# Performance work log

Measured on AMD Instinct MI355X. Metric: run time of the kernel, lower is better.

## Reference

```python
import jax, jax.numpy as jnp
import numpy as np

N_NODES = 50000
N_EDGES = 800000
F_IN = 128
HEADS = 8
HID = 16
EDGE_DIM = 2
EPS = 1e-5
GAT_SLOPE = 0.2   # GATv2Conv default negative_slope
ACT_SLOPE = 0.01  # GATLayer alpha


def setup_inputs() -> dict:
    key = jax.random.key(0)
    ks = jax.random.split(key, 10)
    HC = HEADS * HID
    return {
        "x": jax.random.normal(ks[0], (N_NODES, F_IN), jnp.float32),
        "edge_idx": jax.random.randint(ks[1], (2, N_EDGES), 0, N_NODES, jnp.int32),
        "edge_attr": jax.random.normal(ks[2], (N_EDGES, EDGE_DIM), jnp.float32),
        "Wl": jax.random.normal(ks[3], (F_IN, HC), jnp.float32) * (1.0 / np.sqrt(F_IN)),
        "bl": jnp.zeros((HC,), jnp.float32),
        "Wr": jax.random.normal(ks[4], (F_IN, HC), jnp.float32) * (1.0 / np.sqrt(F_IN)),
        "br": jnp.zeros((HC,), jnp.float32),
        "We": jax.random.normal(ks[5], (EDGE_DIM, HC), jnp.float32) * (1.0 / np.sqrt(EDGE_DIM)),
        "be": jnp.zeros((HC,), jnp.float32),
        "att": jax.random.normal(ks[6], (HEADS, HID), jnp.float32) * (1.0 / np.sqrt(HID)),
        "bias": jnp.zeros((HC,), jnp.float32),
        "gamma": jnp.ones((HC,), jnp.float32),
        "beta": jnp.zeros((HC,), jnp.float32),
    }


def reference(x, edge_idx, edge_attr, Wl, bl, Wr, br, We, be, att, bias, gamma, beta):
    N = x.shape[0]
    H, C = att.shape
    # GATv2: separate source/target linear maps (share_weights=False)
    xl = (x @ Wl + bl).reshape(N, H, C)      # source transform (messages)
    xr = (x @ Wr + br).reshape(N, H, C)      # target transform
    e = (edge_attr @ We + be).reshape(-1, H, C)
    src, dst = edge_idx[0], edge_idx[1]       # edge j -> i
    # edge-wise attention input: [E, H, C]
    m = jax.nn.leaky_relu(xl[src] + xr[dst] + e, GAT_SLOPE)
    logits = jnp.einsum('ehc,hc->eh', m, att)  # [E, H]
    # segment softmax over incoming edges of each target node
    lmax = jax.ops.segment_max(logits, dst, num_segments=N)          # [N, H]
    ex = jnp.exp(logits - lmax[dst])
    denom = jax.ops.segment_sum(ex, dst, num_segments=N)             # [N, H]
    alpha = ex / denom[dst]                                          # [E, H]
    # weighted scatter-aggregate of source messages, concat heads
    out = jax.ops.segment_sum(xl[src] * alpha[:, :, None], dst, num_segments=N)
    out = out.reshape(N, H * C) + bias
    # BatchNorm over nodes (batch statistics), then LeakyReLU(0.01)
    mean = out.mean(axis=0)
    var = out.var(axis=0)
    out = (out - mean) / jnp.sqrt(var + EPS) * gamma + beta
    return jax.nn.leaky_relu(out, ACT_SLOPE)
```

## Files before the change

kernel.cpp:

```cpp
#include <hip/hip_runtime.h>
#include <hip/hip_bf16.h>

#define N_NODES 50000
#define N_EDGES 800000
#define HEADS 8
#define HID 16
#define HC 128

typedef __attribute__((ext_vector_type(8))) short bf16x8;
typedef __attribute__((ext_vector_type(4))) float f32x4;
typedef __attribute__((ext_vector_type(2))) float f32x2;
typedef __attribute__((ext_vector_type(4))) int i32x4;

__device__ __forceinline__ float bf2f(unsigned short u) {
  union { unsigned int i; float f; } v;
  v.i = (unsigned int)u << 16;
  return v.f;
}
__device__ __forceinline__ unsigned short f2bf(float f) {
  __hip_bfloat16 h = __float2bfloat16(f);
  return *(unsigned short*)&h;
}

template <int CTRL>
__device__ __forceinline__ float dpp_addf(float x) {
  const int r = __builtin_amdgcn_update_dpp(0, __float_as_int(x), CTRL, 0xF, 0xF, true);
  return x + __int_as_float(r);
}

__global__ __launch_bounds__(256) void k_prep(
    const int* __restrict__ eidx, const float* __restrict__ Wl,
    const float* __restrict__ Wr, int* __restrict__ deg,
    unsigned short* __restrict__ WcatT) {
  const int b = blockIdx.x;
  if (b < 3125) {
    const int e = b * 256 + threadIdx.x;
    const int d = __builtin_nontemporal_load(eidx + N_EDGES + e);
    atomicAdd(&deg[d], 1);
  } else {
    const int idx = (b - 3125) * 256 + threadIdx.x;
    const int n = idx >> 7, k = idx & 127;
    const float* W = (n < 128) ? Wl : Wr;
    WcatT[idx] = f2bf(W[k * HC + (n & 127)]);
  }
}

__global__ __launch_bounds__(512) void k_gemm_alloc(
    const float* __restrict__ x, const unsigned short* __restrict__ WcatT,
    const float* __restrict__ bl, const float* __restrict__ br,
    unsigned short* __restrict__ xl, unsigned short* __restrict__ xr,
    const int* __restrict__ deg, int* __restrict__ counter,
    int* __restrict__ offs) {
  __shared__ unsigned short As[128 * 136];
  const int t = threadIdx.x;

  if (blockIdx.x >= 391) {
    const int node = (blockIdx.x - 391) * 512 + t;
    const int lane = t & 63;
    const int v = (node < N_NODES) ? deg[node] : 0;
    int incl = v;
#pragma unroll
    for (int d = 1; d < 64; d <<= 1) {
      const int tt = __shfl_up(incl, d);
      if (lane >= d) incl += tt;
    }
    const int total = __shfl(incl, 63);
    int base = 0;
    if (lane == 63) base = atomicAdd(counter, total);
    base = __shfl(base, 63);
    if (node < N_NODES) offs[node] = base + incl - v;
    return;
  }

  const int m0 = blockIdx.x * 128;
#pragma unroll
  for (int it = 0; it < 4; ++it) {
    const int c = t + it * 512;
    const int row = c >> 4;
    const int seg = (c & 15) * 8;
    const int grow = m0 + row;
    float4 a = make_float4(0.f, 0.f, 0.f, 0.f), bb2 = a;
    if (grow < N_NODES) {
      const float4* p = (const float4*)(x + (size_t)grow * 128 + seg);
      a = p[0];
      bb2 = p[1];
    }
    union { unsigned short s[8]; uint4 v; } o;
    o.s[0] = f2bf(a.x);   o.s[1] = f2bf(a.y);
    o.s[2] = f2bf(a.z);   o.s[3] = f2bf(a.w);
    o.s[4] = f2bf(bb2.x); o.s[5] = f2bf(bb2.y);
    o.s[6] = f2bf(bb2.z); o.s[7] = f2bf(bb2.w);
    *(uint4*)(&As[row * 136 + seg]) = o.v;
  }
  __syncthreads();

  const int w = t >> 6, lane = t & 63;
  const int wm = w >> 2, wn = w & 3;
  const int lr = lane & 15, lk = lane >> 4;

  f32x4 acc[4][4];
#pragma unroll
  for (int i = 0; i < 4; ++i)
#pragma unroll
    for (int j = 0; j < 4; ++j) acc[i][j] = (f32x4)(0.f);

  const unsigned short* Wbase = WcatT + (size_t)(wn * 64 + lr) * 128;
#pragma unroll
  for (int ks = 0; ks < 4; ++ks) {
    const int k = ks * 32 + lk * 8;
    bf16x8 bfr[4], afr[4];
#pragma unroll
    for (int ni = 0; ni < 4; ++ni)
      bfr[ni] = *(const bf16x8*)(Wbase + ni * 16 * 128 + k);
#pragma unroll
    for (int mi = 0; mi < 4; ++mi)
      afr[mi] = *(const bf16x8*)(&As[(wm * 64 + mi * 16 + lr) * 136 + k]);
#pragma unroll
    for (int mi = 0; mi < 4; ++mi)
#pragma unroll
      for (int ni = 0; ni < 4; ++ni)
        acc[mi][ni] = __builtin_amdgcn_mfma_f32_16x16x32_bf16(
            afr[mi], bfr[ni], acc[mi][ni], 0, 0, 0);
  }

#pragma unroll
  for (int ni = 0; ni < 4; ++ni) {
    const int gcol = wn * 64 + ni * 16 + lr;
    const bool left = gcol < 128;
    const float bb = left ? bl[gcol] : br[gcol - 128];
    unsigned short* __restrict__ dst = left ? xl : xr;
    const int cc = gcol & 127;
#pragma unroll
    for (int mi = 0; mi < 4; ++mi) {
#pragma unroll
      for (int r = 0; r < 4; ++r) {
        const int grow = m0 + wm * 64 + mi * 16 + lk * 4 + r;
        if (grow < N_NODES) dst[(size_t)grow * HC + cc] = f2bf(acc[mi][ni][r] + bb);
      }
    }
  }
}

__global__ __launch_bounds__(256) void k_scatter(
    const int* __restrict__ eidx, const float* __restrict__ eattr,
    const int* __restrict__ offs, int* __restrict__ cursor,
    i32x4* __restrict__ epack) {
  const int e = blockIdx.x * 256 + threadIdx.x;
  const int src = __builtin_nontemporal_load(eidx + e);
  const int d = __builtin_nontemporal_load(eidx + N_EDGES + e);
  const f32x2 ea = __builtin_nontemporal_load((const f32x2*)eattr + e);
  const int pos = atomicAdd(&cursor[d], 1);
  i32x4 rec;
  rec.x = src;
  rec.y = __float_as_int(ea.x);
  rec.z = __float_as_int(ea.y);
  rec.w = 0;
  __builtin_nontemporal_store(rec, epack + offs[d] + pos);
}

#define LOADB(EP, K)                                   \
  _Pragma("unroll") for (int j = 0; j < 4; ++j) EP[j] = \
      __builtin_nontemporal_load(epack + (K) + j);
#define LOADX(XW, EP)                                                        \
  _Pragma("unroll") for (int j = 0; j < 4; ++j)                              \
      XW[j] = *(const unsigned int*)((const char*)xl +                       \
              (((unsigned)EP[j].x << 8) + lb));
#define EDGE1(EPJ, XWJ)                                                     \
  {                                                                         \
    const float eax = __int_as_float((EPJ).y);                              \
    const float eay = __int_as_float((EPJ).z);                              \
    const float x0 = bf2f((unsigned short)(XWJ));                           \
    const float x1 = bf2f((unsigned short)((XWJ) >> 16));                   \
    float m0 = fmaf(eax, w0a, fmaf(eay, w1a, ca)) + x0;                     \
    float m1 = fmaf(eax, w0b, fmaf(eay, w1b, cb)) + x1;                     \
    m0 = fmaxf(m0, 0.2f * m0);                                              \
    m1 = fmaxf(m1, 0.2f * m1);                                              \
    float p = fmaf(m0, ata, m1 * atb);                                      \
    p = dpp_addf<0xB1>(p);                                                  \
    p = dpp_addf<0x4E>(p);                                                  \
    p = dpp_addf<0x141>(p);                                                 \
    const float exv = __expf(p);                                            \
    dn += exv;                                                              \
    a0 = fmaf(exv, x0, a0);                                                 \
    a1 = fmaf(exv, x1, a1);                                                 \
  }
#define COMPUTE4(EP, XW)                               \
  _Pragma("unroll") for (int j = 0; j < 4; ++j) EDGE1(EP[j], XW[j])

__global__ __launch_bounds__(256) void k_attagg(
    const int* __restrict__ offs, const int* __restrict__ deg,
    const i32x4* __restrict__ epack,
    const unsigned short* __restrict__ xl, const unsigned short* __restrict__ xr,
    const float* __restrict__ We, const float* __restrict__ be,
    const float* __restrict__ att, float* __restrict__ outp,
    float* __restrict__ statsB) {
  __shared__ float ssum[4 * 128];
  __shared__ float ssq[4 * 128];
  const int wave = threadIdx.x >> 6, lane = threadIdx.x & 63;
  const int node = blockIdx.x * 4 + wave;
  const int c0 = lane * 2;
  const unsigned lb = (unsigned)lane << 2;

  const float w0a = We[c0],      w0b = We[c0 + 1];
  const float w1a = We[HC + c0], w1b = We[HC + c0 + 1];
  const float ata = att[c0],     atb = att[c0 + 1];

  const unsigned int xrw =
      __builtin_nontemporal_load((const unsigned int*)(xr + (size_t)node * HC) + lane);
  const float ca = be[c0] + bf2f((unsigned short)xrw);
  const float cb = be[c0 + 1] + bf2f((unsigned short)(xrw >> 16));

  const int beg = offs[node];
  const int dn_e = deg[node];
  const int end = beg + dn_e;
  const int nf = dn_e >> 2;

  float dn = 0.f, a0 = 0.f, a1 = 0.f;

  if (nf >= 1) {
    i32x4 epA[4], epB[4];
    unsigned int xwA[4];
    LOADB(epA, beg)
    LOADX(xwA, epA)
    if (nf >= 2) LOADB(epB, beg + 4)
    for (int b = 0; b + 1 < nf; ++b) {
      unsigned int xwB[4];
      i32x4 epC[4];
      LOADX(xwB, epB)
      if (b + 2 < nf) LOADB(epC, beg + (b + 2) * 4)
      COMPUTE4(epA, xwA)
#pragma unroll
      for (int j = 0; j < 4; ++j) { epA[j] = epB[j]; xwA[j] = xwB[j]; epB[j] = epC[j]; }
    }
    COMPUTE4(epA, xwA)
  }
  for (int k = beg + (nf << 2); k < end; ++k) {
    const i32x4 ep = __builtin_nontemporal_load(epack + k);
    const unsigned int xw =
        *(const unsigned int*)((const char*)xl + (((unsigned)ep.x << 8) + lb));
    EDGE1(ep, xw)
  }

  const float inv = dn > 0.f ? 1.0f / dn : 0.f;
  const float o0 = a0 * inv, o1 = a1 * inv;
  f32x2 o;
  o.x = o0;
  o.y = o1;
  __builtin_nontemporal_store(o, (f32x2*)(outp + (size_t)node * HC) + lane);

  ssum[wave * 128 + c0]     = o0;
  ssum[wave * 128 + c0 + 1] = o1;
  ssq[wave * 128 + c0]      = o0 * o0;
  ssq[wave * 128 + c0 + 1]  = o1 * o1;
  __syncthreads();
  if (threadIdx.x < 128) {
    const int c = threadIdx.x;
    const float s1 = ssum[c] + ssum[128 + c] + ssum[256 + c] + ssum[384 + c];
    const float s2 = ssq[c] + ssq[128 + c] + ssq[256 + c] + ssq[384 + c];
    float* bkt = statsB + (blockIdx.x & 7) * 256;
    atomicAdd(&bkt[c], s1);
    atomicAdd(&bkt[128 + c], s2);
  }
}

__global__ __launch_bounds__(256) void k_bn(const float* __restrict__ statsB,
                                            const float* __restrict__ gamma,
                                            const float* __restrict__ beta,
                                            float* __restrict__ outp) {
  __shared__ float sscale[128], sshift[128];
  const int t = threadIdx.x;
  if (t < 128) {
    float s1 = 0.f, s2 = 0.f;
#pragma unroll
    for (int b = 0; b < 8; ++b) {
      s1 += statsB[b * 256 + t];
      s2 += statsB[b * 256 + 128 + t];
    }
    const float mean = s1 * (1.0f / N_NODES);
    const float var = s2 * (1.0f / N_NODES) - mean * mean;
    const float rstd = rsqrtf(var + 1e-5f);
    const float sc = rstd * gamma[t];
    sscale[t] = sc;
    sshift[t] = beta[t] - mean * sc;
  }
  __syncthreads();
  const size_t base = (size_t)blockIdx.x * 1024 + t * 4;
  float4 v = *(const float4*)(outp + base);
  const int c = (t * 4) & 127;
  v.x = fmaf(v.x, sscale[c],     sshift[c]);
  v.y = fmaf(v.y, sscale[c + 1], sshift[c + 1]);
  v.z = fmaf(v.z, sscale[c + 2], sshift[c + 2]);
  v.w = fmaf(v.w, sscale[c + 3], sshift[c + 3]);
  v.x = fmaxf(v.x, 0.01f * v.x);
  v.y = fmaxf(v.y, 0.01f * v.y);
  v.z = fmaxf(v.z, 0.01f * v.z);
  v.w = fmaxf(v.w, 0.01f * v.w);
  *(float4*)(outp + base) = v;
}

extern "C" void kernel_launch(void* const* d_in, const int* in_sizes, int n_in,
                              void* d_out, int out_size, void* d_ws, size_t ws_size,
                              hipStream_t stream) {
  const float* x     = (const float*)d_in[0];
  const int*   eidx  = (const int*)d_in[1];
  const float* eattr = (const float*)d_in[2];
  const float* Wl    = (const float*)d_in[3];
  const float* bl    = (const float*)d_in[4];
  const float* Wr    = (const float*)d_in[5];
  const float* br    = (const float*)d_in[6];
  const float* We    = (const float*)d_in[7];
  const float* be    = (const float*)d_in[8];
  const float* att   = (const float*)d_in[9];
  const float* gamma = (const float*)d_in[11];
  const float* beta  = (const float*)d_in[12];
  float* out = (float*)d_out;

  char* ws = (char*)d_ws;
  size_t off = 0;
  auto alloc = [&](size_t bytes) {
    size_t o = off;
    off = (off + bytes + 15) & ~size_t(15);
    return o;
  };
  const size_t o_deg   = alloc((size_t)(N_NODES + 1) * 4);
  const size_t o_cur   = alloc((size_t)N_NODES * 4);
  const size_t o_cnt   = alloc(16);
  const size_t o_stats = alloc((size_t)8 * 256 * 4);
  const size_t zero_bytes = off;
  const size_t o_offs = alloc((size_t)(N_NODES + 1) * 4);
  const size_t o_ep   = alloc((size_t)N_EDGES * 16);
  const size_t o_wt   = alloc((size_t)256 * 128 * 2);
  const size_t o_xl   = alloc((size_t)N_NODES * HC * 2);
  const size_t o_xr   = alloc((size_t)N_NODES * HC * 2);
  (void)ws_size; (void)in_sizes; (void)n_in; (void)out_size;

  int*   deg    = (int*)(ws + o_deg);
  int*   cur    = (int*)(ws + o_cur);
  int*   cnt    = (int*)(ws + o_cnt);
  float* statsB = (float*)(ws + o_stats);
  int*   offs   = (int*)(ws + o_offs);
  i32x4* epack  = (i32x4*)(ws + o_ep);
  unsigned short* WcatT = (unsigned short*)(ws + o_wt);
  unsigned short* xl    = (unsigned short*)(ws + o_xl);
  unsigned short* xr    = (unsigned short*)(ws + o_xr);

  hipMemsetAsync(ws, 0, zero_bytes, stream);

  k_prep<<<3253, 256, 0, stream>>>(eidx, Wl, Wr, deg, WcatT);
  k_gemm_alloc<<<489, 512, 0, stream>>>(x, WcatT, bl, br, xl, xr, deg, cnt, offs);
  k_scatter<<<3125, 256, 0, stream>>>(eidx, eattr, offs, cur, epack);
  k_attagg<<<12500, 256, 0, stream>>>(offs, deg, epack, xl, xr, We, be, att, out,
                                      statsB);
  k_bn<<<6250, 256, 0, stream>>>(statsB, gamma, beta, out);
}
```

Measured before the change: 299.5 us.

## Pack edge records to 8 bytes with bf16 attrs, deepen gather prefetch, use exp2

```diff
diff --git a/kernel.cpp b/kernel.cpp
--- a/kernel.cpp
+++ b/kernel.cpp
@@ -10,7 +10,7 @@
 typedef __attribute__((ext_vector_type(8))) short bf16x8;
 typedef __attribute__((ext_vector_type(4))) float f32x4;
 typedef __attribute__((ext_vector_type(2))) float f32x2;
-typedef __attribute__((ext_vector_type(4))) int i32x4;
+typedef __attribute__((ext_vector_type(2))) int i32x2;
 
 __device__ __forceinline__ float bf2f(unsigned short u) {
   union { unsigned int i; float f; } v;
@@ -144,17 +144,15 @@
 __global__ __launch_bounds__(256) void k_scatter(
     const int* __restrict__ eidx, const float* __restrict__ eattr,
     const int* __restrict__ offs, int* __restrict__ cursor,
-    i32x4* __restrict__ epack) {
+    i32x2* __restrict__ epack) {
   const int e = blockIdx.x * 256 + threadIdx.x;
   const int src = __builtin_nontemporal_load(eidx + e);
   const int d = __builtin_nontemporal_load(eidx + N_EDGES + e);
   const f32x2 ea = __builtin_nontemporal_load((const f32x2*)eattr + e);
   const int pos = atomicAdd(&cursor[d], 1);
-  i32x4 rec;
+  i32x2 rec;
   rec.x = src;
-  rec.y = __float_as_int(ea.x);
-  rec.z = __float_as_int(ea.y);
-  rec.w = 0;
+  rec.y = (int)((unsigned)f2bf(ea.x) | ((unsigned)f2bf(ea.y) << 16));
   __builtin_nontemporal_store(rec, epack + offs[d] + pos);
 }
 
@@ -167,8 +165,9 @@
               (((unsigned)EP[j].x << 8) + lb));
 #define EDGE1(EPJ, XWJ)                                                     \
   {                                                                         \
-    const float eax = __int_as_float((EPJ).y);                              \
-    const float eay = __int_as_float((EPJ).z);                              \
+    const unsigned eu = (unsigned)(EPJ).y;                                  \
+    const float eax = bf2f((unsigned short)eu);                             \
+    const float eay = bf2f((unsigned short)(eu >> 16));                     \
     const float x0 = bf2f((unsigned short)(XWJ));                           \
     const float x1 = bf2f((unsigned short)((XWJ) >> 16));                   \
     float m0 = fmaf(eax, w0a, fmaf(eay, w1a, ca)) + x0;                     \
@@ -179,17 +178,19 @@
     p = dpp_addf<0xB1>(p);                                                  \
     p = dpp_addf<0x4E>(p);                                                  \
     p = dpp_addf<0x141>(p);                                                 \
-    const float exv = __expf(p);                                            \
+    const float exv = exp2f(p);                                             \
     dn += exv;                                                              \
     a0 = fmaf(exv, x0, a0);                                                 \
     a1 = fmaf(exv, x1, a1);                                                 \
   }
 #define COMPUTE4(EP, XW)                               \
   _Pragma("unroll") for (int j = 0; j < 4; ++j) EDGE1(EP[j], XW[j])
+#define SHIFT4(A, B)                                   \
+  _Pragma("unroll") for (int j = 0; j < 4; ++j) A[j] = B[j];
 
 __global__ __launch_bounds__(256) void k_attagg(
     const int* __restrict__ offs, const int* __restrict__ deg,
-    const i32x4* __restrict__ epack,
+    const i32x2* __restrict__ epack,
     const unsigned short* __restrict__ xl, const unsigned short* __restrict__ xr,
     const float* __restrict__ We, const float* __restrict__ be,
     const float* __restrict__ att, float* __restrict__ outp,
@@ -203,7 +204,8 @@
 
   const float w0a = We[c0],      w0b = We[c0 + 1];
   const float w1a = We[HC + c0], w1b = We[HC + c0 + 1];
-  const float ata = att[c0],     atb = att[c0 + 1];
+  const float LOG2E = 1.4426950408889634f;
+  const float ata = att[c0] * LOG2E, atb = att[c0 + 1] * LOG2E;
 
   const unsigned int xrw =
       __builtin_nontemporal_load((const unsigned int*)(xr + (size_t)node * HC) + lane);
@@ -218,24 +220,27 @@
   float dn = 0.f, a0 = 0.f, a1 = 0.f;
 
   if (nf >= 1) {
-    i32x4 epA[4], epB[4];
-    unsigned int xwA[4];
-    LOADB(epA, beg)
-    LOADX(xwA, epA)
-    if (nf >= 2) LOADB(epB, beg + 4)
-    for (int b = 0; b + 1 < nf; ++b) {
-      unsigned int xwB[4];
-      i32x4 epC[4];
-      LOADX(xwB, epB)
-      if (b + 2 < nf) LOADB(epC, beg + (b + 2) * 4)
-      COMPUTE4(epA, xwA)
-#pragma unroll
-      for (int j = 0; j < 4; ++j) { epA[j] = epB[j]; xwA[j] = xwB[j]; epB[j] = epC[j]; }
-    }
-    COMPUTE4(epA, xwA)
+    i32x2 ep0[4], ep1[4], ep2[4];
+    unsigned int xw0[4], xw1[4];
+    LOADB(ep0, beg)
+    if (nf >= 2) LOADB(ep1, beg + 4)
+    if (nf >= 3) LOADB(ep2, beg + 8)
+    LOADX(xw0, ep0)
+    if (nf >= 2) LOADX(xw1, ep1)
+    for (int b = 0; b + 2 < nf; ++b) {
+      unsigned int xw2[4];
+      i32x2 ep3[4];
+      LOADX(xw2, ep2)
+      if (b + 3 < nf) LOADB(ep3, beg + (b + 3) * 4)
+      COMPUTE4(ep0, xw0)
+      SHIFT4(ep0, ep1) SHIFT4(ep1, ep2) SHIFT4(ep2, ep3)
+      SHIFT4(xw0, xw1) SHIFT4(xw1, xw2)
+    }
+    COMPUTE4(ep0, xw0)
+    if (nf >= 2) COMPUTE4(ep1, xw1)
   }
   for (int k = beg + (nf << 2); k < end; ++k) {
-    const i32x4 ep = __builtin_nontemporal_load(epack + k);
+    const i32x2 ep = __builtin_nontemporal_load(epack + k);
     const unsigned int xw =
         *(const unsigned int*)((const char*)xl + (((unsigned)ep.x << 8) + lb));
     EDGE1(ep, xw)
@@ -285,7 +290,7 @@
   }
   __syncthreads();
   const size_t base = (size_t)blockIdx.x * 1024 + t * 4;
-  float4 v = *(const float4*)(outp + base);
+  f32x4 v = __builtin_nontemporal_load((const f32x4*)(outp + base));
   const int c = (t * 4) & 127;
   v.x = fmaf(v.x, sscale[c],     sshift[c]);
   v.y = fmaf(v.y, sscale[c + 1], sshift[c + 1]);
@@ -295,7 +300,7 @@
   v.y = fmaxf(v.y, 0.01f * v.y);
   v.z = fmaxf(v.z, 0.01f * v.z);
   v.w = fmaxf(v.w, 0.01f * v.w);
-  *(float4*)(outp + base) = v;
+  __builtin_nontemporal_store(v, (f32x4*)(outp + base));
 }
 
 extern "C" void kernel_launch(void* const* d_in, const int* in_sizes, int n_in,
@@ -328,7 +333,7 @@
   const size_t o_stats = alloc((size_t)8 * 256 * 4);
   const size_t zero_bytes = off;
   const size_t o_offs = alloc((size_t)(N_NODES + 1) * 4);
-  const size_t o_ep   = alloc((size_t)N_EDGES * 16);
+  const size_t o_ep   = alloc((size_t)N_EDGES * 8);
   const size_t o_wt   = alloc((size_t)256 * 128 * 2);
   const size_t o_xl   = alloc((size_t)N_NODES * HC * 2);
   const size_t o_xr   = alloc((size_t)N_NODES * HC * 2);
@@ -339,12 +344,12 @@
   int*   cnt    = (int*)(ws + o_cnt);
   float* statsB = (float*)(ws + o_stats);
   int*   offs   = (int*)(ws + o_offs);
-  i32x4* epack  = (i32x4*)(ws + o_ep);
+  i32x2* epack  = (i32x2*)(ws + o_ep);
   unsigned short* WcatT = (unsigned short*)(ws + o_wt);
   unsigned short* xl    = (unsigned short*)(ws + o_xl);
   unsigned short* xr    = (unsigned short*)(ws + o_xr);
 
-  hipMemsetAsync(ws, 0, zero_bytes, stream);
+  (void)hipMemsetAsync(ws, 0, zero_bytes, stream);
 
   k_prep<<<3253, 256, 0, stream>>>(eidx, Wl, Wr, deg, WcatT);
   k_gemm_alloc<<<489, 512, 0, stream>>>(x, WcatT, bl, br, xl, xr, deg, cnt, offs);
```

Result: faster. 289.8 us (-3.2%).
